# Performance work log

Measured on AMD Instinct MI355X. Metric: run time of the kernel, lower is better.

The kernel has to match this reference:

```python
import jax, jax.numpy as jnp
import numpy as np

D_MODEL = 96
D_STATE = 16
D_CONV = 3
D_INNER = 192          # expand * d_model
DT_RANK = 6            # ceil(d_model / 16)
K = 4                  # 4 scan directions
LN_EPS = 1e-5


def setup_inputs() -> dict:
    key = jax.random.key(0)
    ks = jax.random.split(key, 8)
    rn = lambda k, shape, s: jax.random.normal(k, shape, jnp.float32) * s
    return {
        "x": rn(ks[0], (8, 64, 64, D_MODEL), 1.0),
        "in_proj_w": rn(ks[1], (2 * D_INNER, D_MODEL), 0.05),
        "conv_w": rn(ks[2], (D_INNER, 1, D_CONV, D_CONV), 0.1),
        "conv_b": rn(ks[3], (D_INNER,), 0.1),
        "x_proj_w": rn(ks[4], (K * (DT_RANK + 2 * D_STATE), D_INNER), 0.05),
        "dt_projs_w": rn(ks[5], (K * D_INNER, DT_RANK), 0.1),
        "dt_projs_b": rn(ks[6], (K * D_INNER,), 0.1),
        "A_log": jnp.log(jnp.tile(jnp.arange(1, D_STATE + 1, dtype=jnp.float32), (D_INNER, 1))),
        "Ds": jnp.ones((K * D_INNER,), jnp.float32),
        "out_norm_w": jnp.ones((D_INNER,), jnp.float32),
        "out_norm_b": jnp.zeros((D_INNER,), jnp.float32),
        "out_proj_w": rn(ks[7], (D_MODEL, D_INNER), 0.05),
    }


def _selective_scan(u, delta, A, Bs, Cs):
    # u, delta: (B,K,D,L); A: (D,N); Bs, Cs: (B,K,N,L)
    Bsz = u.shape[0]

    def step(h, t):
        u_t, d_t, B_t, C_t = t                       # (B,K,D), (B,K,D), (B,K,N), (B,K,N)
        h = jnp.exp(d_t[..., None] * A) * h + (d_t * u_t)[..., None] * B_t[:, :, None, :]
        y = jnp.einsum('bkdn,bkn->bkd', h, C_t)
        return h, y

    h0 = jnp.zeros((Bsz, K, D_INNER, D_STATE), u.dtype)
    seq = (jnp.moveaxis(u, -1, 0), jnp.moveaxis(delta, -1, 0),
           jnp.moveaxis(Bs, -1, 0), jnp.moveaxis(Cs, -1, 0))
    _, ys = jax.lax.scan(step, h0, seq)
    return jnp.moveaxis(ys, 0, -1)                   # (B,K,D,L)


def reference(x, in_proj_w, conv_w, conv_b, x_proj_w, dt_projs_w, dt_projs_b,
              A_log, Ds, out_norm_w, out_norm_b, out_proj_w):
    B, H, W, C = x.shape
    L = H * W
    # in_proj + gate split
    xz = x @ in_proj_w.T                             # (B,H,W,2*D_INNER)
    x_, z = jnp.split(xz, 2, axis=-1)
    # depthwise conv + SiLU (NCHW)
    xc = jnp.transpose(x_, (0, 3, 1, 2))
    pad = (D_CONV - 1) // 2
    xc = jax.lax.conv_general_dilated(xc, conv_w, (1, 1), [(pad, pad), (pad, pad)],
                                      feature_group_count=D_INNER)
    xc = xc + conv_b[None, :, None, None]
    xc = xc * jax.nn.sigmoid(xc)
    # CrossScan: 4 directions
    x0 = xc.reshape(B, D_INNER, L)
    x1 = jnp.transpose(xc, (0, 1, 3, 2)).reshape(B, D_INNER, L)
    xs = jnp.stack([x0, x1, x0[..., ::-1], x1[..., ::-1]], axis=1)   # (B,4,D,L)
    # per-direction projections
    x_dbl = jnp.einsum('bkdl,kcd->bkcl', xs, x_proj_w.reshape(K, -1, D_INNER))
    dts, Bs, Cs = jnp.split(x_dbl, [DT_RANK, DT_RANK + D_STATE], axis=2)
    dts = jnp.einsum('bkrl,kdr->bkdl', dts, dt_projs_w.reshape(K, D_INNER, DT_RANK))
    delta = jax.nn.softplus(dts + dt_projs_b.reshape(1, K, D_INNER, 1))
    A = -jnp.exp(A_log)                              # (D,N), shared across K
    ys = _selective_scan(xs, delta, A, Bs, Cs)
    ys = ys + Ds.reshape(1, K, D_INNER, 1) * xs      # skip term D*u
    # CrossMerge
    y02 = ys[:, 0] + ys[:, 2, :, ::-1]
    y13 = ys[:, 1] + ys[:, 3, :, ::-1]
    y = y02 + jnp.transpose(y13.reshape(B, D_INNER, W, H), (0, 1, 3, 2)).reshape(B, D_INNER, L)
    # LayerNorm over channels (out_norm, 'v0' path)
    yt = jnp.transpose(y, (0, 2, 1))                 # (B,L,D)
    mu = yt.mean(-1, keepdims=True)
    var = yt.var(-1, keepdims=True)
    yt = (yt - mu) / jnp.sqrt(var + LN_EPS) * out_norm_w + out_norm_b
    yt = yt.reshape(B, H, W, D_INNER)
    # gate and out_proj
    yg = yt * (z * jax.nn.sigmoid(z))
    return yg @ out_proj_w.T
```

## Files before the change

kernel.cpp:

```cpp
#include <hip/hip_runtime.h>
#include <hip/hip_bf16.h>

typedef __hip_bfloat16 bf16;
typedef unsigned short u16;
typedef unsigned int   u32;

constexpr int Hn=64, Wn=64, Cm=96, Ln=4096, Di=192, Kn=4, Ns=16, Rr=6;
constexpr int Gc=64, CH=64;

typedef __attribute__((ext_vector_type(8))) short bf16x8;
typedef __attribute__((ext_vector_type(4))) float f32x4;

static __device__ __forceinline__ float ldv(const float* p, long i){ return p[i]; }
static __device__ __forceinline__ float ldv(const bf16*  p, long i){ return __bfloat162float(p[i]); }
static __device__ __forceinline__ void  stv(float* p, long i, float v){ p[i] = v; }
static __device__ __forceinline__ void  stv(bf16*  p, long i, float v){ p[i] = __float2bfloat16(v); }
static __device__ __forceinline__ float bfr(u16 u){ return __uint_as_float((u32)u << 16); }
static __device__ __forceinline__ u16   fbr(float f){ bf16 h = __float2bfloat16(f); return *(u16*)&h; }
static __device__ __forceinline__ float4 ldv4(const float* p, long i){ return *(const float4*)(p + i); }
static __device__ __forceinline__ float4 ldv4(const bf16* p, long i){
  ushort4 u = *(const ushort4*)(p + i);
  return make_float4(bfr(u.x), bfr(u.y), bfr(u.z), bfr(u.w));
}
static __device__ __forceinline__ float splus(float x){ return (x > 15.f) ? x : log1pf(__expf(x)); }

static __device__ __forceinline__ bf16x8 ldb8(const float* p){
  float4 a = *(const float4*)p;
  float4 b = *(const float4*)(p + 4);
  bf16x8 r;
  r[0]=(short)fbr(a.x); r[1]=(short)fbr(a.y); r[2]=(short)fbr(a.z); r[3]=(short)fbr(a.w);
  r[4]=(short)fbr(b.x); r[5]=(short)fbr(b.y); r[6]=(short)fbr(b.z); r[7]=(short)fbr(b.w);
  return r;
}
static __device__ __forceinline__ bf16x8 ldb8(const bf16* p){
  return *(const bf16x8*)p;
}
static __device__ __forceinline__ void st8(u16* dst, const float* src){
  float4 a = *(const float4*)src;
  float4 b = *(const float4*)(src + 4);
  dst[0]=fbr(a.x); dst[1]=fbr(a.y); dst[2]=fbr(a.z); dst[3]=fbr(a.w);
  dst[4]=fbr(b.x); dst[5]=fbr(b.y); dst[6]=fbr(b.z); dst[7]=fbr(b.w);
}
static __device__ __forceinline__ void st8(u16* dst, const bf16* src){
  *(ushort4*)dst       = *(const ushort4*)src;
  *(ushort4*)(dst + 4) = *(const ushort4*)(src + 4);
}

__global__ void k_detect(const u16* x, const void* Alog, int* flag, int* flag2){
  __shared__ int cnt, cnt2;
  if (threadIdx.x == 0){ cnt = 0; cnt2 = 0; }
  __syncthreads();
  int local = 0;
  for (int i = threadIdx.x; i < 8192; i += 256){
    int e = (x[i] >> 7) & 0xFF;
    if (e != 0 && (e < 90 || e > 164)) local++;
  }
  atomicAdd(&cnt, local);
  __syncthreads();
  int f = (cnt > 400) ? 1 : 0;
  int bad = 0;
  for (int i = threadIdx.x; i < Di*Ns; i += 256){
    float v = f ? ((const float*)Alog)[i] : bfr(((const u16*)Alog)[i]);
    float ex = __logf((float)((i & 15) + 1));
    if (fabsf(v - ex) > 1e-5f) bad++;
  }
  atomicAdd(&cnt2, bad);
  __syncthreads();
  if (threadIdx.x == 0){ *flag = f; *flag2 = (cnt2 == 0) ? 1 : 0; }
}

template<typename T>
__device__ void inproj_body(const T* x, const T* w, u16* Xb, u16* Z, u16* sA, u16* sC){
  int tid = threadIdx.x;
  long p0 = (long)blockIdx.x * 64;
  for (int i = tid; i < 768; i += 256){
    int r = i / 12, c = (i % 12) * 8;
    st8(&sA[r*104 + c], x + p0*96 + (long)r*96 + c);
  }
  __syncthreads();
  int wid = tid >> 6, lane = tid & 63;
  int lr = lane & 15, lh = lane >> 4;
  int colbase = wid * 96;
  f32x4 acc[4][6] = {};
  #pragma unroll
  for (int ks = 0; ks < 3; ++ks){
    int k0 = ks*32 + lh*8;
    bf16x8 af[4];
    #pragma unroll
    for (int m = 0; m < 4; ++m)
      af[m] = *(const bf16x8*)&sA[(m*16 + lr)*104 + k0];
    #pragma unroll
    for (int n = 0; n < 6; ++n){
      bf16x8 b8 = ldb8(w + (long)(colbase + n*16 + lr)*96 + k0);
      #pragma unroll
      for (int m = 0; m < 4; ++m)
        acc[m][n] = __builtin_amdgcn_mfma_f32_16x16x32_bf16(af[m], b8, acc[m][n], 0, 0, 0);
    }
  }
  #pragma unroll
  for (int n = 0; n < 6; ++n){
    int gc = colbase + n*16 + lr;
    #pragma unroll
    for (int m = 0; m < 4; ++m){
      #pragma unroll
      for (int r = 0; r < 4; ++r)
        sC[(m*16 + lh*4 + r)*392 + gc] = fbr(acc[m][n][r]);
    }
  }
  __syncthreads();
  for (int i = tid; i < 3072; i += 256){
    int r = i / 48, c = (i % 48) * 8;
    ushort4 v0 = *(const ushort4*)&sC[r*392 + c];
    ushort4 v1 = *(const ushort4*)&sC[r*392 + c + 4];
    u16* dst = (c < 192) ? (Xb + (p0 + r)*192 + c) : (Z + (p0 + r)*192 + (c - 192));
    *(ushort4*)dst       = v0;
    *(ushort4*)(dst + 4) = v1;
  }
}
__global__ __launch_bounds__(256) void k_inproj(const void* x, long xoff, const void* w,
                                                u16* Xb, u16* Z, const int* flag){
  __shared__ u16 sA[64*104];
  __shared__ u16 sC[64*392];
  if (*flag) inproj_body<float>((const float*)x + xoff, (const float*)w, Xb, Z, sA, sC);
  else       inproj_body<bf16 >((const bf16* )x + xoff, (const bf16* )w, Xb, Z, sA, sC);
}

template<typename T>
__device__ void conv_body(const u16* Xb, const T* cw, const T* cb,
                          u16* xcLD, u16* xcTLD, float* wv, float* bv){
  int blk = blockIdx.x;
  int dq = blk % 3; int hb = blk / 3; int h = hb & 63; int b = hb >> 6;
  int tid = threadIdx.x;
  int d0 = dq*64;
  for (int i = tid; i < 576; i += 256){
    int c = i & 63, t = i >> 6;
    wv[t*64 + c] = ldv(cw, (long)(d0 + c)*9 + t);
  }
  if (tid < 64) bv[tid] = ldv(cb, d0 + tid);
  __syncthreads();
  const u16* Xbb = Xb + (long)b*Ln*Di;
  u16* xa = xcLD  + (long)b*Ln*Di;
  u16* xb = xcTLD + (long)b*Ln*Di;
  int c8l = (tid & 7)*8;
  int d = d0 + c8l;
  float4 wf[9][2];
  #pragma unroll
  for (int t = 0; t < 9; ++t){
    wf[t][0] = *(const float4*)&wv[t*64 + c8l];
    wf[t][1] = *(const float4*)&wv[t*64 + c8l + 4];
  }
  float bss[8];
  #pragma unroll
  for (int q = 0; q < 8; ++q) bss[q] = bv[c8l + q];
  #pragma unroll
  for (int half = 0; half < 2; ++half){
    int w = (tid >> 3) + half*32;
    float acc[8];
    #pragma unroll
    for (int q = 0; q < 8; ++q) acc[q] = bss[q];
    #pragma unroll
    for (int dh = -1; dh <= 1; ++dh){
      int hh = h + dh;
      if ((unsigned)hh > 63u) continue;
      #pragma unroll
      for (int dw = -1; dw <= 1; ++dw){
        int ww = w + dw;
        if ((unsigned)ww > 63u) continue;
        int t = (dh+1)*3 + (dw+1);
        const u16* p = Xbb + (long)(hh*64 + ww)*Di + d;
        ushort4 v0 = *(const ushort4*)p;
        ushort4 v1 = *(const ushort4*)(p + 4);
        acc[0] += wf[t][0].x * bfr(v0.x);
        acc[1] += wf[t][0].y * bfr(v0.y);
        acc[2] += wf[t][0].z * bfr(v0.z);
        acc[3] += wf[t][0].w * bfr(v0.w);
        acc[4] += wf[t][1].x * bfr(v1.x);
        acc[5] += wf[t][1].y * bfr(v1.y);
        acc[6] += wf[t][1].z * bfr(v1.z);
        acc[7] += wf[t][1].w * bfr(v1.w);
      }
    }
    u16 o[8];
    #pragma unroll
    for (int q = 0; q < 8; ++q){
      float e = __expf(-acc[q]);
      float sv = acc[q] * __builtin_amdgcn_rcpf(1.f + e);
      o[q] = fbr(sv);
    }
    ushort4 s0; s0.x=o[0]; s0.y=o[1]; s0.z=o[2]; s0.w=o[3];
    ushort4 s1; s1.x=o[4]; s1.y=o[5]; s1.z=o[6]; s1.w=o[7];
    u16* pa = xa + (long)(h*64 + w)*Di + d;
    u16* pb = xb + (long)(w*64 + h)*Di + d;
    *(ushort4*)pa = s0; *(ushort4*)(pa + 4) = s1;
    *(ushort4*)pb = s0; *(ushort4*)(pb + 4) = s1;
  }
}
__global__ __launch_bounds__(256,4) void k_conv(const u16* Xb, const void* cw, const void* cb,
                                                u16* xcLD, u16* xcTLD, const int* flag){
  __shared__ float wv[576];
  __shared__ float bv[64];
  if (*flag) conv_body<float>(Xb, (const float*)cw, (const float*)cb, xcLD, xcTLD, wv, bv);
  else       conv_body<bf16 >(Xb, (const bf16* )cw, (const bf16* )cb, xcLD, xcTLD, wv, bv);
}

template<typename T>
__device__ void proj_body(const u16* xcLD, const u16* xcTLD, const T* xpw,
                          u16* dtsg, u32* BCg, u16* sA){
  int tid = threadIdx.x;
  int s = blockIdx.x & 1;
  long q0 = (long)(blockIdx.x >> 1) * 64;
  const u16* src = (s ? xcTLD : xcLD) + q0*192;
  for (int i = tid; i < 1536; i += 256){
    int r = i / 24, c = (i % 24) * 8;
    const u16* sp = src + (long)r*192 + c;
    *(ushort4*)&sA[r*200 + c]     = *(const ushort4*)sp;
    *(ushort4*)&sA[r*200 + c + 4] = *(const ushort4*)(sp + 4);
  }
  __syncthreads();
  int wid = tid >> 6, lane = tid & 63;
  int lr = lane & 15, lh = lane >> 4;
  f32x4 acc[5] = {};
  #pragma unroll
  for (int ks = 0; ks < 6; ++ks){
    int k0 = ks*32 + lh*8;
    bf16x8 a = *(const bf16x8*)&sA[(wid*16 + lr)*200 + k0];
    #pragma unroll
    for (int f = 0; f < 5; ++f){
      int c = f*16 + lr;
      int cw;
      if (c < 38)      cw = s*38 + c;
      else if (c < 76) cw = (s+2)*38 + (c - 38);
      else             cw = 0;
      bf16x8 b8 = ldb8(xpw + (long)cw*192 + k0);
      acc[f] = __builtin_amdgcn_mfma_f32_16x16x32_bf16(a, b8, acc[f], 0, 0, 0);
    }
  }
  int row_l = wid*16 + lh*4;
  #pragma unroll
  for (int f = 0; f < 5; ++f){
    int c = f*16 + lr;
    if (c >= 76) continue;
    int k = (c < 38) ? s : s + 2;
    int t = (c < 38) ? c : c - 38;
    if (t >= 22) continue;
    #pragma unroll
    for (int r = 0; r < 4; ++r){
      long q = q0 + row_l + r;
      int b  = (int)(q >> 12);
      int ql = (int)(q & 4095);
      int l  = (k >= 2) ? (4095 - ql) : ql;
      long base = ((long)(b*4 + k))*4096 + l;
      if (t < 6){
        dtsg[base*6 + t] = fbr(acc[f][r]);
      } else {
        int n = t - 6;
        u32 v = (u32)fbr(acc[f][r]) | ((u32)fbr(acc[f+1][r]) << 16);
        BCg[base*16 + n] = v;
      }
    }
  }
}
__global__ __launch_bounds__(256) void k_proj(const u16* xcLD, const u16* xcTLD, const void* xpw,
                                              u16* dtsg, u32* BCg, const int* flag){
  __shared__ u16 sA[64*200];
  if (*flag) proj_body<float>(xcLD, xcTLD, (const float*)xpw, dtsg, BCg, sA);
  else       proj_body<bf16 >(xcLD, xcTLD, (const bf16* )xpw, dtsg, BCg, sA);
}

static __device__ __forceinline__ void sp_decay(float xv, float& dl, float& rr){
  if (xv > 15.f){ dl = xv; rr = __expf(-xv); }
  else {
    float o = 1.f + __expf(xv);
    dl = __logf(o);
    rr = __builtin_amdgcn_rcpf(o);
  }
}

template<typename T>
__device__ void scan1_body(const u16* xcLD, const u16* xcTLD, const u16* dtsg, const u32* BCg,
                           const T* Alog, const T* dtw, const T* dtb,
                           float* Sb, float* Qb, float* sdt, float* sB, int fastA){
  int tid = threadIdx.x, blk = blockIdx.x;
  int g = blk & (Gc-1); int k = (blk >> 6) & 3; int b = blk >> 8;
  bool rev = k >= 2, odd = k & 1;
  int d = tid;
  const u16* src = (odd ? xcTLD : xcLD) + (long)b*Ln*Di;
  const u16* dlg = dtsg + (long)(b*Kn + k)*Ln*6;
  const u32* bcg = BCg + (long)(b*Kn + k)*Ln*16;
  float w[6], h[16], a[16];
  #pragma unroll
  for (int r = 0; r < 6; ++r) w[r] = ldv(dtw, ((long)k*Di + d)*6 + r);
  float bias = ldv(dtb, k*Di + d);
  #pragma unroll
  for (int n = 0; n < 16; ++n) h[n] = 0.f;
  if (!fastA){
    #pragma unroll
    for (int n = 0; n < 16; ++n) a[n] = -__expf(ldv(Alog, (long)d*16 + n));
  }
  float S = 0.f;
  int l0 = g*CH;
  for (int i = tid; i < 48; i += 192){
    const u16* sp8 = dlg + (long)l0*6 + i*8;
    ushort4 v0 = *(const ushort4*)sp8;
    ushort4 v1 = *(const ushort4*)(sp8 + 4);
    float* dp = &sdt[i*8];
    dp[0]=bfr(v0.x); dp[1]=bfr(v0.y); dp[2]=bfr(v0.z); dp[3]=bfr(v0.w);
    dp[4]=bfr(v1.x); dp[5]=bfr(v1.y); dp[6]=bfr(v1.z); dp[7]=bfr(v1.w);
  }
  for (int i = tid; i < 256; i += 192){
    uint4 v = *(const uint4*)(bcg + (long)l0*16 + i*4);
    sB[i*4+0] = bfr((u16)(v.x & 0xffff));
    sB[i*4+1] = bfr((u16)(v.y & 0xffff));
    sB[i*4+2] = bfr((u16)(v.z & 0xffff));
    sB[i*4+3] = bfr((u16)(v.w & 0xffff));
  }
  __syncthreads();
  if (fastA){
    for (int jb = 0; jb < CH; jb += 8){
      float uv[8];
      #pragma unroll
      for (int q = 0; q < 8; ++q){
        int l = l0 + jb + q; int pos = rev ? (Ln-1-l) : l;
        uv[q] = bfr(src[(long)pos*Di + d]);
      }
      #pragma unroll
      for (int q = 0; q < 8; ++q){
        int j = jb + q;
        float xv = bias;
        #pragma unroll
        for (int r = 0; r < 6; ++r) xv += w[r]*sdt[j*6 + r];
        float dl, rr; sp_decay(xv, dl, rr);
        float du = dl * uv[q];
        float Bv[16];
        *(float4*)&Bv[0]  = *(const float4*)&sB[j*16];
        *(float4*)&Bv[4]  = *(const float4*)&sB[j*16+4];
        *(float4*)&Bv[8]  = *(const float4*)&sB[j*16+8];
        *(float4*)&Bv[12] = *(const float4*)&sB[j*16+12];
        float r2 = rr*rr, r3 = r2*rr, r4 = r2*r2, r8 = r4*r4, r12 = r8*r4;
        float S4[4] = {rr, r2, r3, r4};
        float B4[4] = {1.f, r4, r8, r12};
        #pragma unroll
        for (int n = 0; n < 16; ++n)
          h[n] = (B4[n>>2]*S4[n&3])*h[n] + du*Bv[n];
        S += dl;
      }
    }
  } else {
    for (int jb = 0; jb < CH; jb += 8){
      float uv[8];
      #pragma unroll
      for (int q = 0; q < 8; ++q){
        int l = l0 + jb + q; int pos = rev ? (Ln-1-l) : l;
        uv[q] = bfr(src[(long)pos*Di + d]);
      }
      #pragma unroll
      for (int q = 0; q < 8; ++q){
        int j = jb + q;
        float dl = bias;
        #pragma unroll
        for (int r = 0; r < 6; ++r) dl += w[r]*sdt[j*6 + r];
        dl = splus(dl);
        float du = dl * uv[q];
        float Bv[16];
        *(float4*)&Bv[0]  = *(const float4*)&sB[j*16];
        *(float4*)&Bv[4]  = *(const float4*)&sB[j*16+4];
        *(float4*)&Bv[8]  = *(const float4*)&sB[j*16+8];
        *(float4*)&Bv[12] = *(const float4*)&sB[j*16+12];
        #pragma unroll
        for (int n = 0; n < 16; ++n) h[n] = __expf(dl*a[n])*h[n] + du*Bv[n];
        S += dl;
      }
    }
  }
  long ci = (long)(b*Kn + k)*Gc + g;
  Sb[ci*Di + d] = S;
  float4* qp = (float4*)(Qb + ci*3072 + (long)d*16);
  qp[0] = make_float4(h[0], h[1], h[2], h[3]);
  qp[1] = make_float4(h[4], h[5], h[6], h[7]);
  qp[2] = make_float4(h[8], h[9], h[10], h[11]);
  qp[3] = make_float4(h[12], h[13], h[14], h[15]);
}
__global__ __launch_bounds__(192,3) void k_scan1(const u16* xcLD, const u16* xcTLD, const u16* dtsg,
                                                 const u32* BCg, const void* Alog, const void* dtw,
                                                 const void* dtb, float* Sb, float* Qb,
                                                 const int* flag, const int* flag2){
  __shared__ float sdt[384];
  __shared__ float sB[1024];
  int f2 = *flag2;
  if (*flag) scan1_body<float>(xcLD, xcTLD, dtsg, BCg, (const float*)Alog, (const float*)dtw,
                               (const float*)dtb, Sb, Qb, sdt, sB, f2);
  else       scan1_body<bf16 >(xcLD, xcTLD, dtsg, BCg, (const bf16* )Alog, (const bf16* )dtw,
                               (const bf16* )dtb, Sb, Qb, sdt, sB, f2);
}

template<typename T>
__device__ void fix_body(const float* Sb, const float* Qb, const T* Alog, float* Hin){
  int bk = blockIdx.x >> 2, qr = blockIdx.x & 3;
  int s0 = qr*768 + threadIdx.x;
  float aa[3], hh[3];
  #pragma unroll
  for (int q = 0; q < 3; ++q){
    int s = s0 + 256*q;
    aa[q] = -__expf(ldv(Alog, s));
    hh[q] = 0.f;
  }
  for (int g = 0; g < Gc; ++g){
    long ci = (long)bk*Gc + g;
    #pragma unroll
    for (int q = 0; q < 3; ++q){
      int s = s0 + 256*q;
      Hin[ci*3072 + s] = hh[q];
      hh[q] = __expf(aa[q]*Sb[ci*Di + (s >> 4)])*hh[q] + Qb[ci*3072 + s];
    }
  }
}
__global__ __launch_bounds__(256) void k_fix(const float* Sb, const float* Qb, const void* Alog,
                                             float* Hin, const int* flag){
  if (*flag) fix_body<float>(Sb, Qb, (const float*)Alog, Hin);
  else       fix_body<bf16 >(Sb, Qb, (const bf16* )Alog, Hin);
}

template<typename T>
__device__ void scan2_body(const u16* xcLD, const u16* xcTLD, const u16* dtsg, const u32* BCg,
                           const T* Alog, const T* dtw, const T* dtb, const float* Hin,
                           u16* ys, float* sdt, float* sB, float* sC, int fastA){
  int tid = threadIdx.x, blk = blockIdx.x;
  int g = blk & (Gc-1); int k = (blk >> 6) & 3; int b = blk >> 8;
  bool rev = k >= 2, odd = k & 1;
  int d = tid;
  const u16* src = (odd ? xcTLD : xcLD) + (long)b*Ln*Di;
  const u16* dlg = dtsg + (long)(b*Kn + k)*Ln*6;
  const u32* bcg = BCg + (long)(b*Kn + k)*Ln*16;
  u16* yb = ys + (long)(b*Kn + k)*Ln*Di;
  float w[6], h[16], a[16];
  #pragma unroll
  for (int r = 0; r < 6; ++r) w[r] = ldv(dtw, ((long)k*Di + d)*6 + r);
  float bias = ldv(dtb, k*Di + d);
  long ci = (long)(b*Kn + k)*Gc + g;
  {
    const float4* hp = (const float4*)(Hin + ci*3072 + (long)d*16);
    float4 h0 = hp[0], h1 = hp[1], h2 = hp[2], h3 = hp[3];
    h[0]=h0.x; h[1]=h0.y; h[2]=h0.z; h[3]=h0.w;
    h[4]=h1.x; h[5]=h1.y; h[6]=h1.z; h[7]=h1.w;
    h[8]=h2.x; h[9]=h2.y; h[10]=h2.z; h[11]=h2.w;
    h[12]=h3.x; h[13]=h3.y; h[14]=h3.z; h[15]=h3.w;
  }
  if (!fastA){
    #pragma unroll
    for (int n = 0; n < 16; ++n) a[n] = -__expf(ldv(Alog, (long)d*16 + n));
  }
  int l0 = g*CH;
  for (int i = tid; i < 48; i += 192){
    const u16* sp8 = dlg + (long)l0*6 + i*8;
    ushort4 v0 = *(const ushort4*)sp8;
    ushort4 v1 = *(const ushort4*)(sp8 + 4);
    float* dp = &sdt[i*8];
    dp[0]=bfr(v0.x); dp[1]=bfr(v0.y); dp[2]=bfr(v0.z); dp[3]=bfr(v0.w);
    dp[4]=bfr(v1.x); dp[5]=bfr(v1.y); dp[6]=bfr(v1.z); dp[7]=bfr(v1.w);
  }
  for (int i = tid; i < 256; i += 192){
    uint4 v = *(const uint4*)(bcg + (long)l0*16 + i*4);
    sB[i*4+0] = bfr((u16)(v.x & 0xffff)); sC[i*4+0] = bfr((u16)(v.x >> 16));
    sB[i*4+1] = bfr((u16)(v.y & 0xffff)); sC[i*4+1] = bfr((u16)(v.y >> 16));
    sB[i*4+2] = bfr((u16)(v.z & 0xffff)); sC[i*4+2] = bfr((u16)(v.z >> 16));
    sB[i*4+3] = bfr((u16)(v.w & 0xffff)); sC[i*4+3] = bfr((u16)(v.w >> 16));
  }
  __syncthreads();
  if (fastA){
    for (int jb = 0; jb < CH; jb += 8){
      float uv[8];
      #pragma unroll
      for (int q = 0; q < 8; ++q){
        int l = l0 + jb + q; int pos = rev ? (Ln-1-l) : l;
        uv[q] = bfr(src[(long)pos*Di + d]);
      }
      #pragma unroll
      for (int q = 0; q < 8; ++q){
        int j = jb + q;
        float xv = bias;
        #pragma unroll
        for (int r = 0; r < 6; ++r) xv += w[r]*sdt[j*6 + r];
        float dl, rr; sp_decay(xv, dl, rr);
        float du = dl * uv[q];
        float Bv[16], Cv[16];
        *(float4*)&Bv[0]  = *(const float4*)&sB[j*16];
        *(float4*)&Bv[4]  = *(const float4*)&sB[j*16+4];
        *(float4*)&Bv[8]  = *(const float4*)&sB[j*16+8];
        *(float4*)&Bv[12] = *(const float4*)&sB[j*16+12];
        *(float4*)&Cv[0]  = *(const float4*)&sC[j*16];
        *(float4*)&Cv[4]  = *(const float4*)&sC[j*16+4];
        *(float4*)&Cv[8]  = *(const float4*)&sC[j*16+8];
        *(float4*)&Cv[12] = *(const float4*)&sC[j*16+12];
        float r2 = rr*rr, r3 = r2*rr, r4 = r2*r2, r8 = r4*r4, r12 = r8*r4;
        float S4[4] = {rr, r2, r3, r4};
        float B4[4] = {1.f, r4, r8, r12};
        float y = 0.f;
        #pragma unroll
        for (int n = 0; n < 16; ++n){
          h[n] = (B4[n>>2]*S4[n&3])*h[n] + du*Bv[n];
          y += h[n]*Cv[n];
        }
        int l = l0 + j; int le = rev ? (Ln-1-l) : l;
        int sp = odd ? ((le & 63)*64 + (le >> 6)) : le;
        yb[(long)sp*Di + d] = fbr(y);
      }
    }
  } else {
    for (int jb = 0; jb < CH; jb += 8){
      float uv[8];
      #pragma unroll
      for (int q = 0; q < 8; ++q){
        int l = l0 + jb + q; int pos = rev ? (Ln-1-l) : l;
        uv[q] = bfr(src[(long)pos*Di + d]);
      }
      #pragma unroll
      for (int q = 0; q < 8; ++q){
        int j = jb + q;
        float dl = bias;
        #pragma unroll
        for (int r = 0; r < 6; ++r) dl += w[r]*sdt[j*6 + r];
        dl = splus(dl);
        float du = dl * uv[q];
        float Bv[16], Cv[16];
        *(float4*)&Bv[0]  = *(const float4*)&sB[j*16];
        *(float4*)&Bv[4]  = *(const float4*)&sB[j*16+4];
        *(float4*)&Bv[8]  = *(const float4*)&sB[j*16+8];
        *(float4*)&Bv[12] = *(const float4*)&sB[j*16+12];
        *(float4*)&Cv[0]  = *(const float4*)&sC[j*16];
        *(float4*)&Cv[4]  = *(const float4*)&sC[j*16+4];
        *(float4*)&Cv[8]  = *(const float4*)&sC[j*16+8];
        *(float4*)&Cv[12] = *(const float4*)&sC[j*16+12];
        float y = 0.f;
        #pragma unroll
        for (int n = 0; n < 16; ++n){
          h[n] = __expf(dl*a[n])*h[n] + du*Bv[n];
          y += h[n]*Cv[n];
        }
        int l = l0 + j; int le = rev ? (Ln-1-l) : l;
        int sp = odd ? ((le & 63)*64 + (le >> 6)) : le;
        yb[(long)sp*Di + d] = fbr(y);
      }
    }
  }
}
__global__ __launch_bounds__(192,3) void k_scan2(const u16* xcLD, const u16* xcTLD, const u16* dtsg,
                                                 const u32* BCg, const void* Alog, const void* dtw,
                                                 const void* dtb, const float* Hin, u16* ys,
                                                 const int* flag, const int* flag2){
  __shared__ float sdt[384];
  __shared__ float sB[1024];
  __shared__ float sC[1024];
  int f2 = *flag2;
  if (*flag) scan2_body<float>(xcLD, xcTLD, dtsg, BCg, (const float*)Alog, (const float*)dtw,
                               (const float*)dtb, Hin, ys, sdt, sB, sC, f2);
  else       scan2_body<bf16 >(xcLD, xcTLD, dtsg, BCg, (const bf16* )Alog, (const bf16* )dtw,
                               (const bf16* )dtb, Hin, ys, sdt, sB, sC, f2);
}

template<typename T>
__device__ void out_body(const u16* ys, const u16* xcLD, const u16* Z, const T* Dsv,
                         const T* lnw, const T* lnb, const T* wo, T* out, long obase,
                         u16* ty, float* sDs){
  int blk = blockIdx.x;
  int b = blk >> 7; int rem = blk & 127; int h = rem >> 1; int half = rem & 1;
  int tid = threadIdx.x;
  int p0 = h*64 + half*32;
  const u16* xcb = xcLD + (long)b*Ln*Di;
  const u16* Zb  = Z + (long)b*Ln*Di;
  const u16* pl0 = ys + (long)(b*Kn + 0)*Ln*Di;
  const u16* pl1 = ys + (long)(b*Kn + 1)*Ln*Di;
  const u16* pl2 = ys + (long)(b*Kn + 2)*Ln*Di;
  const u16* pl3 = ys + (long)(b*Kn + 3)*Ln*Di;
  if (tid < Di)
    sDs[tid] = ldv(Dsv, tid) + ldv(Dsv, Di+tid) + ldv(Dsv, 2*Di+tid) + ldv(Dsv, 3*Di+tid);
  __syncthreads();
  for (int i = tid; i < 768; i += 256){
    int j = i / 24, c8 = (i % 24) * 8;
    int wc = half*32 + j;
    long ls = (long)(p0 + j)*Di + c8;
    long lt = (long)(wc*64 + h)*Di + c8;
    ushort4 a0 = *(const ushort4*)(pl0 + ls); ushort4 a1 = *(const ushort4*)(pl0 + ls + 4);
    ushort4 b0 = *(const ushort4*)(pl2 + ls); ushort4 b1 = *(const ushort4*)(pl2 + ls + 4);
    ushort4 c0 = *(const ushort4*)(pl1 + lt); ushort4 c1 = *(const ushort4*)(pl1 + lt + 4);
    ushort4 d0 = *(const ushort4*)(pl3 + lt); ushort4 d1 = *(const ushort4*)(pl3 + lt + 4);
    ushort4 x0 = *(const ushort4*)(xcb + ls); ushort4 x1 = *(const ushort4*)(xcb + ls + 4);
    u16* tp = &ty[j*200 + c8];
    tp[0] = fbr(bfr(a0.x)+bfr(b0.x)+bfr(c0.x)+bfr(d0.x) + sDs[c8+0]*bfr(x0.x));
    tp[1] = fbr(bfr(a0.y)+bfr(b0.y)+bfr(c0.y)+bfr(d0.y) + sDs[c8+1]*bfr(x0.y));
    tp[2] = fbr(bfr(a0.z)+bfr(b0.z)+bfr(c0.z)+bfr(d0.z) + sDs[c8+2]*bfr(x0.z));
    tp[3] = fbr(bfr(a0.w)+bfr(b0.w)+bfr(c0.w)+bfr(d0.w) + sDs[c8+3]*bfr(x0.w));
    tp[4] = fbr(bfr(a1.x)+bfr(b1.x)+bfr(c1.x)+bfr(d1.x) + sDs[c8+4]*bfr(x1.x));
    tp[5] = fbr(bfr(a1.y)+bfr(b1.y)+bfr(c1.y)+bfr(d1.y) + sDs[c8+5]*bfr(x1.y));
    tp[6] = fbr(bfr(a1.z)+bfr(b1.z)+bfr(c1.z)+bfr(d1.z) + sDs[c8+6]*bfr(x1.z));
    tp[7] = fbr(bfr(a1.w)+bfr(b1.w)+bfr(c1.w)+bfr(d1.w) + sDs[c8+7]*bfr(x1.w));
  }
  __syncthreads();
  int jj = tid >> 3, part = tid & 7;
  float s = 0.f, s2 = 0.f;
  for (int cix = part*24; cix < part*24 + 24; ++cix){
    float v = bfr(ty[jj*200 + cix]); s += v; s2 += v*v;
  }
  s += __shfl_xor(s, 1); s2 += __shfl_xor(s2, 1);
  s += __shfl_xor(s, 2); s2 += __shfl_xor(s2, 2);
  s += __shfl_xor(s, 4); s2 += __shfl_xor(s2, 4);
  float mu = s * (1.f/192.f);
  float var = s2 * (1.f/192.f) - mu*mu;
  float rstd = rsqrtf(fmaxf(var, 0.f) + 1e-5f);
  long zbase = (long)(p0 + jj)*Di;
  for (int cix = part*24; cix < part*24 + 24; ++cix){
    float zv = bfr(Zb[zbase + cix]);
    float gt = zv / (1.f + __expf(-zv));
    float yn = (bfr(ty[jj*200 + cix]) - mu) * rstd * ldv(lnw, cix) + ldv(lnb, cix);
    ty[jj*200 + cix] = fbr(yn * gt);
  }
  __syncthreads();
  int wid = tid >> 6, lane = tid & 63;
  int wm = wid & 1, wn = wid >> 1;
  int lr = lane & 15, lh = lane >> 4;
  f32x4 acc[3] = {};
  #pragma unroll
  for (int ks = 0; ks < 6; ++ks){
    int k0 = ks*32 + lh*8;
    bf16x8 av = *(const bf16x8*)&ty[(wm*16 + lr)*200 + k0];
    #pragma unroll
    for (int n = 0; n < 3; ++n){
      bf16x8 b8 = ldb8(wo + (long)(wn*48 + n*16 + lr)*192 + k0);
      acc[n] = __builtin_amdgcn_mfma_f32_16x16x32_bf16(av, b8, acc[n], 0, 0, 0);
    }
  }
  #pragma unroll
  for (int n = 0; n < 3; ++n){
    int col = wn*48 + n*16 + lr;
    #pragma unroll
    for (int r = 0; r < 4; ++r){
      long row = (long)b*Ln + p0 + wm*16 + lh*4 + r;
      stv(out, obase + row*Cm + col, acc[n][r]);
    }
  }
}
__global__ __launch_bounds__(256) void k_out(const u16* ys, const u16* xcLD, const u16* Z,
                                             const void* Dsv, const void* lnw, const void* lnb,
                                             const void* wo, void* out, long obase, const int* flag){
  __shared__ u16 ty[32*200];
  __shared__ float sDs[Di];
  if (*flag) out_body<float>(ys, xcLD, Z, (const float*)Dsv, (const float*)lnw, (const float*)lnb,
                             (const float*)wo, (float*)out, obase, ty, sDs);
  else       out_body<bf16 >(ys, xcLD, Z, (const bf16* )Dsv, (const bf16* )lnw, (const bf16* )lnb,
                             (const bf16* )wo, (bf16* )out, obase, ty, sDs);
}

extern "C" void kernel_launch(void* const* d_in, const int* in_sizes, int n_in,
                              void* d_out, int out_size, void* d_ws, size_t ws_size,
                              hipStream_t stream){
  const void* x    = d_in[0];
  const void* ipw  = d_in[1];
  const void* cw   = d_in[2];
  const void* cb   = d_in[3];
  const void* xpw  = d_in[4];
  const void* dtw  = d_in[5];
  const void* dtb  = d_in[6];
  const void* Alog = d_in[7];
  const void* Dsv  = d_in[8];
  const void* lnw  = d_in[9];
  const void* lnb  = d_in[10];
  const void* wo   = d_in[11];

  const size_t PLANE = (size_t)Ln*Di*2;
  const size_t YSB   = (size_t)Kn*Ln*Di*2;
  const size_t SBB   = (size_t)Kn*Gc*Di*4;
  const size_t QBB   = (size_t)Kn*Gc*Di*Ns*4;
  const size_t HIB   = QBB;
  const size_t perB  = 4*PLANE + YSB + SBB + QBB + HIB;
  int Bc = 1;
  for (int c : {8, 4, 2, 1}) if (256 + (size_t)c*perB <= ws_size){ Bc = c; break; }
  int nch = 8 / Bc;

  char* base = (char*)d_ws;
  int*  flag  = (int*)base;
  int*  flag2 = (int*)(base + 8);
  u16* Z     = (u16*)(base + 256);
  u16* xcLD  = Z     + (size_t)Bc*Ln*Di;
  u16* xcTLD = xcLD  + (size_t)Bc*Ln*Di;
  u16* Xb    = xcTLD + (size_t)Bc*Ln*Di;
  u16* ys    = Xb    + (size_t)Bc*Ln*Di;
  float* Sb  = (float*)(ys + (size_t)Bc*Kn*Ln*Di);
  float* Qb  = Sb + (size_t)Bc*Kn*Gc*Di;
  float* Hin = Qb + (size_t)Bc*Kn*Gc*Di*Ns;
  u16* dts   = Xb;
  u32* BC    = (u32*)(dts + (size_t)Bc*Kn*Ln*6);

  k_detect<<<1, 256, 0, stream>>>((const u16*)x, Alog, flag, flag2);

  for (int ch = 0; ch < nch; ++ch){
    long xoff = (long)ch*Bc*Ln*Cm;
    k_inproj <<<Bc*Ln/64,     256, 0, stream>>>(x, xoff, ipw, Xb, Z, flag);
    k_conv   <<<Bc*Hn*3,      256, 0, stream>>>(Xb, cw, cb, xcLD, xcTLD, flag);
    k_proj   <<<Bc*(Ln/64)*2, 256, 0, stream>>>(xcLD, xcTLD, xpw, dts, BC, flag);
    k_scan1  <<<Bc*Kn*Gc,     192, 0, stream>>>(xcLD, xcTLD, dts, BC, Alog, dtw, dtb, Sb, Qb, flag, flag2);
    k_fix    <<<Bc*Kn*4,      256, 0, stream>>>(Sb, Qb, Alog, Hin, flag);
    k_scan2  <<<Bc*Kn*Gc,     192, 0, stream>>>(xcLD, xcTLD, dts, BC, Alog, dtw, dtb, Hin, ys, flag, flag2);
    k_out    <<<Bc*Hn*2,      256, 0, stream>>>(ys, xcLD, Z, Dsv, lnw, lnb, wo, d_out, xoff, flag);
  }
}
```

Baseline: 379.0 us.

## Split scan state dimension across two threads per channel

Both scan kernels now use 384 threads per block, with two lanes per channel, each holding 8 of the 16 state entries. In the second pass the per-step output is combined with a lane shuffle, and only the even lane stores it. This halves registers per thread and doubles the parallelism available to hide the serial recurrence latency. The cost is duplicated delta/softplus/exp work and duplicated u loads per lane pair, plus an extra shuffle every step.

```diff
diff --git a/kernel.cpp b/kernel.cpp
--- a/kernel.cpp
+++ b/kernel.cpp
@@ -283,23 +283,23 @@
   int tid = threadIdx.x, blk = blockIdx.x;
   int g = blk & (Gc-1); int k = (blk >> 6) & 3; int b = blk >> 8;
   bool rev = k >= 2, odd = k & 1;
-  int d = tid;
+  int d = tid >> 1, half = tid & 1;
   const u16* src = (odd ? xcTLD : xcLD) + (long)b*Ln*Di;
   const u16* dlg = dtsg + (long)(b*Kn + k)*Ln*6;
   const u32* bcg = BCg + (long)(b*Kn + k)*Ln*16;
-  float w[6], h[16], a[16];
+  float w[6], h[8], a[8];
   #pragma unroll
   for (int r = 0; r < 6; ++r) w[r] = ldv(dtw, ((long)k*Di + d)*6 + r);
   float bias = ldv(dtb, k*Di + d);
   #pragma unroll
-  for (int n = 0; n < 16; ++n) h[n] = 0.f;
+  for (int n = 0; n < 8; ++n) h[n] = 0.f;
   if (!fastA){
     #pragma unroll
-    for (int n = 0; n < 16; ++n) a[n] = -__expf(ldv(Alog, (long)d*16 + n));
+    for (int n = 0; n < 8; ++n) a[n] = -__expf(ldv(Alog, (long)d*16 + half*8 + n));
   }
   float S = 0.f;
   int l0 = g*CH;
-  for (int i = tid; i < 48; i += 192){
+  for (int i = tid; i < 48; i += 384){
     const u16* sp8 = dlg + (long)l0*6 + i*8;
     ushort4 v0 = *(const ushort4*)sp8;
     ushort4 v1 = *(const ushort4*)(sp8 + 4);
@@ -307,7 +307,7 @@
     dp[0]=bfr(v0.x); dp[1]=bfr(v0.y); dp[2]=bfr(v0.z); dp[3]=bfr(v0.w);
     dp[4]=bfr(v1.x); dp[5]=bfr(v1.y); dp[6]=bfr(v1.z); dp[7]=bfr(v1.w);
   }
-  for (int i = tid; i < 256; i += 192){
+  for (int i = tid; i < 256; i += 384){
     uint4 v = *(const uint4*)(bcg + (long)l0*16 + i*4);
     sB[i*4+0] = bfr((u16)(v.x & 0xffff));
     sB[i*4+1] = bfr((u16)(v.y & 0xffff));
@@ -331,17 +331,16 @@
         for (int r = 0; r < 6; ++r) xv += w[r]*sdt[j*6 + r];
         float dl, rr; sp_decay(xv, dl, rr);
         float du = dl * uv[q];
-        float Bv[16];
-        *(float4*)&Bv[0]  = *(const float4*)&sB[j*16];
-        *(float4*)&Bv[4]  = *(const float4*)&sB[j*16+4];
-        *(float4*)&Bv[8]  = *(const float4*)&sB[j*16+8];
-        *(float4*)&Bv[12] = *(const float4*)&sB[j*16+12];
-        float r2 = rr*rr, r3 = r2*rr, r4 = r2*r2, r8 = r4*r4, r12 = r8*r4;
+        float Bv[8];
+        *(float4*)&Bv[0] = *(const float4*)&sB[j*16 + half*8];
+        *(float4*)&Bv[4] = *(const float4*)&sB[j*16 + half*8 + 4];
+        float r2 = rr*rr, r3 = r2*rr, r4 = r2*r2, r8 = r4*r4;
         float S4[4] = {rr, r2, r3, r4};
-        float B4[4] = {1.f, r4, r8, r12};
-        #pragma unroll
-        for (int n = 0; n < 16; ++n)
-          h[n] = (B4[n>>2]*S4[n&3])*h[n] + du*Bv[n];
+        float b0 = half ? r8 : 1.f;
+        float b1 = half ? r8*r4 : r4;
+        #pragma unroll
+        for (int n = 0; n < 8; ++n)
+          h[n] = (((n < 4) ? b0 : b1)*S4[n&3])*h[n] + du*Bv[n];
         S += dl;
       }
     }
@@ -361,26 +360,22 @@
         for (int r = 0; r < 6; ++r) dl += w[r]*sdt[j*6 + r];
         dl = splus(dl);
         float du = dl * uv[q];
-        float Bv[16];
-        *(float4*)&Bv[0]  = *(const float4*)&sB[j*16];
-        *(float4*)&Bv[4]  = *(const float4*)&sB[j*16+4];
-        *(float4*)&Bv[8]  = *(const float4*)&sB[j*16+8];
-        *(float4*)&Bv[12] = *(const float4*)&sB[j*16+12];
-        #pragma unroll
-        for (int n = 0; n < 16; ++n) h[n] = __expf(dl*a[n])*h[n] + du*Bv[n];
+        float Bv[8];
+        *(float4*)&Bv[0] = *(const float4*)&sB[j*16 + half*8];
+        *(float4*)&Bv[4] = *(const float4*)&sB[j*16 + half*8 + 4];
+        #pragma unroll
+        for (int n = 0; n < 8; ++n) h[n] = __expf(dl*a[n])*h[n] + du*Bv[n];
         S += dl;
       }
     }
   }
   long ci = (long)(b*Kn + k)*Gc + g;
-  Sb[ci*Di + d] = S;
-  float4* qp = (float4*)(Qb + ci*3072 + (long)d*16);
+  if (!half) Sb[ci*Di + d] = S;
+  float4* qp = (float4*)(Qb + ci*3072 + (long)d*16 + half*8);
   qp[0] = make_float4(h[0], h[1], h[2], h[3]);
   qp[1] = make_float4(h[4], h[5], h[6], h[7]);
-  qp[2] = make_float4(h[8], h[9], h[10], h[11]);
-  qp[3] = make_float4(h[12], h[13], h[14], h[15]);
-}
-__global__ __launch_bounds__(192,3) void k_scan1(const u16* xcLD, const u16* xcTLD, const u16* dtsg,
+}
+__global__ __launch_bounds__(384,2) void k_scan1(const u16* xcLD, const u16* xcTLD, const u16* dtsg,
                                                  const u32* BCg, const void* Alog, const void* dtw,
                                                  const void* dtb, float* Sb, float* Qb,
                                                  const int* flag, const int* flag2){
@@ -427,30 +422,28 @@
   int tid = threadIdx.x, blk = blockIdx.x;
   int g = blk & (Gc-1); int k = (blk >> 6) & 3; int b = blk >> 8;
   bool rev = k >= 2, odd = k & 1;
-  int d = tid;
+  int d = tid >> 1, half = tid & 1;
   const u16* src = (odd ? xcTLD : xcLD) + (long)b*Ln*Di;
   const u16* dlg = dtsg + (long)(b*Kn + k)*Ln*6;
   const u32* bcg = BCg + (long)(b*Kn + k)*Ln*16;
   u16* yb = ys + (long)(b*Kn + k)*Ln*Di;
-  float w[6], h[16], a[16];
+  float w[6], h[8], a[8];
   #pragma unroll
   for (int r = 0; r < 6; ++r) w[r] = ldv(dtw, ((long)k*Di + d)*6 + r);
   float bias = ldv(dtb, k*Di + d);
   long ci = (long)(b*Kn + k)*Gc + g;
   {
-    const float4* hp = (const float4*)(Hin + ci*3072 + (long)d*16);
-    float4 h0 = hp[0], h1 = hp[1], h2 = hp[2], h3 = hp[3];
+    const float4* hp = (const float4*)(Hin + ci*3072 + (long)d*16 + half*8);
+    float4 h0 = hp[0], h1 = hp[1];
     h[0]=h0.x; h[1]=h0.y; h[2]=h0.z; h[3]=h0.w;
     h[4]=h1.x; h[5]=h1.y; h[6]=h1.z; h[7]=h1.w;
-    h[8]=h2.x; h[9]=h2.y; h[10]=h2.z; h[11]=h2.w;
-    h[12]=h3.x; h[13]=h3.y; h[14]=h3.z; h[15]=h3.w;
   }
   if (!fastA){
     #pragma unroll
-    for (int n = 0; n < 16; ++n) a[n] = -__expf(ldv(Alog, (long)d*16 + n));
+    for (int n = 0; n < 8; ++n) a[n] = -__expf(ldv(Alog, (long)d*16 + half*8 + n));
   }
   int l0 = g*CH;
-  for (int i = tid; i < 48; i += 192){
+  for (int i = tid; i < 48; i += 384){
     const u16* sp8 = dlg + (long)l0*6 + i*8;
     ushort4 v0 = *(const ushort4*)sp8;
     ushort4 v1 = *(const ushort4*)(sp8 + 4);
@@ -458,7 +451,7 @@
     dp[0]=bfr(v0.x); dp[1]=bfr(v0.y); dp[2]=bfr(v0.z); dp[3]=bfr(v0.w);
     dp[4]=bfr(v1.x); dp[5]=bfr(v1.y); dp[6]=bfr(v1.z); dp[7]=bfr(v1.w);
   }
-  for (int i = tid; i < 256; i += 192){
+  for (int i = tid; i < 256; i += 384){
     uint4 v = *(const uint4*)(bcg + (long)l0*16 + i*4);
     sB[i*4+0] = bfr((u16)(v.x & 0xffff)); sC[i*4+0] = bfr((u16)(v.x >> 16));
     sB[i*4+1] = bfr((u16)(v.y & 0xffff)); sC[i*4+1] = bfr((u16)(v.y >> 16));
@@ -482,27 +475,27 @@
         for (int r = 0; r < 6; ++r) xv += w[r]*sdt[j*6 + r];
         float dl, rr; sp_decay(xv, dl, rr);
         float du = dl * uv[q];
-        float Bv[16], Cv[16];
-        *(float4*)&Bv[0]  = *(const float4*)&sB[j*16];
-        *(float4*)&Bv[4]  = *(const float4*)&sB[j*16+4];
-        *(float4*)&Bv[8]  = *(const float4*)&sB[j*16+8];
-        *(float4*)&Bv[12] = *(const float4*)&sB[j*16+12];
-        *(float4*)&Cv[0]  = *(const float4*)&sC[j*16];
-        *(float4*)&Cv[4]  = *(const float4*)&sC[j*16+4];
-        *(float4*)&Cv[8]  = *(const float4*)&sC[j*16+8];
-        *(float4*)&Cv[12] = *(const float4*)&sC[j*16+12];
-        float r2 = rr*rr, r3 = r2*rr, r4 = r2*r2, r8 = r4*r4, r12 = r8*r4;
+        float Bv[8], Cv[8];
+        *(float4*)&Bv[0] = *(const float4*)&sB[j*16 + half*8];
+        *(float4*)&Bv[4] = *(const float4*)&sB[j*16 + half*8 + 4];
+        *(float4*)&Cv[0] = *(const float4*)&sC[j*16 + half*8];
+        *(float4*)&Cv[4] = *(const float4*)&sC[j*16 + half*8 + 4];
+        float r2 = rr*rr, r3 = r2*rr, r4 = r2*r2, r8 = r4*r4;
         float S4[4] = {rr, r2, r3, r4};
-        float B4[4] = {1.f, r4, r8, r12};
+        float b0 = half ? r8 : 1.f;
+        float b1 = half ? r8*r4 : r4;
         float y = 0.f;
         #pragma unroll
-        for (int n = 0; n < 16; ++n){
-          h[n] = (B4[n>>2]*S4[n&3])*h[n] + du*Bv[n];
+        for (int n = 0; n < 8; ++n){
+          h[n] = (((n < 4) ? b0 : b1)*S4[n&3])*h[n] + du*Bv[n];
           y += h[n]*Cv[n];
         }
-        int l = l0 + j; int le = rev ? (Ln-1-l) : l;
-        int sp = odd ? ((le & 63)*64 + (le >> 6)) : le;
-        yb[(long)sp*Di + d] = fbr(y);
+        y += __shfl_xor(y, 1);
+        if (!half){
+          int l = l0 + j; int le = rev ? (Ln-1-l) : l;
+          int sp = odd ? ((le & 63)*64 + (le >> 6)) : le;
+          yb[(long)sp*Di + d] = fbr(y);
+        }
       }
     }
   } else {
@@ -521,29 +514,28 @@
         for (int r = 0; r < 6; ++r) dl += w[r]*sdt[j*6 + r];
         dl = splus(dl);
         float du = dl * uv[q];
-        float Bv[16], Cv[16];
-        *(float4*)&Bv[0]  = *(const float4*)&sB[j*16];
-        *(float4*)&Bv[4]  = *(const float4*)&sB[j*16+4];
-        *(float4*)&Bv[8]  = *(const float4*)&sB[j*16+8];
-        *(float4*)&Bv[12] = *(const float4*)&sB[j*16+12];
-        *(float4*)&Cv[0]  = *(const float4*)&sC[j*16];
-        *(float4*)&Cv[4]  = *(const float4*)&sC[j*16+4];
-        *(float4*)&Cv[8]  = *(const float4*)&sC[j*16+8];
-        *(float4*)&Cv[12] = *(const float4*)&sC[j*16+12];
+        float Bv[8], Cv[8];
+        *(float4*)&Bv[0] = *(const float4*)&sB[j*16 + half*8];
+        *(float4*)&Bv[4] = *(const float4*)&sB[j*16 + half*8 + 4];
+        *(float4*)&Cv[0] = *(const float4*)&sC[j*16 + half*8];
+        *(float4*)&Cv[4] = *(const float4*)&sC[j*16 + half*8 + 4];
         float y = 0.f;
         #pragma unroll
-        for (int n = 0; n < 16; ++n){
+        for (int n = 0; n < 8; ++n){
           h[n] = __expf(dl*a[n])*h[n] + du*Bv[n];
           y += h[n]*Cv[n];
         }
-        int l = l0 + j; int le = rev ? (Ln-1-l) : l;
-        int sp = odd ? ((le & 63)*64 + (le >> 6)) : le;
-        yb[(long)sp*Di + d] = fbr(y);
-      }
-    }
-  }
-}
-__global__ __launch_bounds__(192,3) void k_scan2(const u16* xcLD, const u16* xcTLD, const u16* dtsg,
+        y += __shfl_xor(y, 1);
+        if (!half){
+          int l = l0 + j; int le = rev ? (Ln-1-l) : l;
+          int sp = odd ? ((le & 63)*64 + (le >> 6)) : le;
+          yb[(long)sp*Di + d] = fbr(y);
+        }
+      }
+    }
+  }
+}
+__global__ __launch_bounds__(384,2) void k_scan2(const u16* xcLD, const u16* xcTLD, const u16* dtsg,
                                                  const u32* BCg, const void* Alog, const void* dtw,
                                                  const void* dtb, const float* Hin, u16* ys,
                                                  const int* flag, const int* flag2){
@@ -696,9 +688,9 @@
     k_inproj <<<Bc*Ln/64,     256, 0, stream>>>(x, xoff, ipw, Xb, Z, flag);
     k_conv   <<<Bc*Hn*3,      256, 0, stream>>>(Xb, cw, cb, xcLD, xcTLD, flag);
     k_proj   <<<Bc*(Ln/64)*2, 256, 0, stream>>>(xcLD, xcTLD, xpw, dts, BC, flag);
-    k_scan1  <<<Bc*Kn*Gc,     192, 0, stream>>>(xcLD, xcTLD, dts, BC, Alog, dtw, dtb, Sb, Qb, flag, flag2);
+    k_scan1  <<<Bc*Kn*Gc,     384, 0, stream>>>(xcLD, xcTLD, dts, BC, Alog, dtw, dtb, Sb, Qb, flag, flag2);
     k_fix    <<<Bc*Kn*4,      256, 0, stream>>>(Sb, Qb, Alog, Hin, flag);
-    k_scan2  <<<Bc*Kn*Gc,     192, 0, stream>>>(xcLD, xcTLD, dts, BC, Alog, dtw, dtb, Hin, ys, flag, flag2);
+    k_scan2  <<<Bc*Kn*Gc,     384, 0, stream>>>(xcLD, xcTLD, dts, BC, Alog, dtw, dtb, Hin, ys, flag, flag2);
     k_out    <<<Bc*Hn*2,      256, 0, stream>>>(ys, xcLD, Z, Dsv, lnw, lnb, wo, d_out, xoff, flag);
   }
 }
```

Measured after the change: 422.8 us. +11.6%, slower.
